# Kernel tuning notes

Hardware: AMD Instinct MI355X
Metric: run time of the kernel (lower is better)

The kernel has to match this reference:

```python
import jax, jax.numpy as jnp
import numpy as np
import math

D_MODEL = 768
NUM_HEADS = 12
D_K = D_MODEL // NUM_HEADS
B, S = 4, 2048


def setup_inputs() -> dict:
    key = jax.random.key(0)
    ks = jax.random.split(key, 11)
    s = 1.0 / math.sqrt(D_MODEL)
    inp = {
        "q": jax.random.normal(ks[0], (B, S, D_MODEL), jnp.float32),
        "k": jax.random.normal(ks[1], (B, S, D_MODEL), jnp.float32),
        "v": jax.random.normal(ks[2], (B, S, D_MODEL), jnp.float32),
        "w_q": jax.random.normal(ks[3], (D_MODEL, D_MODEL), jnp.float32) * s,
        "b_q": jax.random.normal(ks[4], (D_MODEL,), jnp.float32) * s,
        "w_k": jax.random.normal(ks[5], (D_MODEL, D_MODEL), jnp.float32) * s,
        "b_k": jax.random.normal(ks[6], (D_MODEL,), jnp.float32) * s,
        "w_v": jax.random.normal(ks[7], (D_MODEL, D_MODEL), jnp.float32) * s,
        "b_v": jax.random.normal(ks[8], (D_MODEL,), jnp.float32) * s,
        "w_o": jax.random.normal(ks[9], (D_MODEL, D_MODEL), jnp.float32) * s,
        "b_o": jax.random.normal(ks[10], (D_MODEL,), jnp.float32) * s,
    }
    return inp


def reference(q, k, v, w_q, b_q, w_k, b_k, w_v, b_v, w_o, b_o):
    b = q.shape[0]
    # Linear projections (torch Linear: x @ W.T + b), reshape to [B,H,S,d_k]
    def proj(x, w, bias):
        y = x @ w.T + bias
        return y.reshape(b, -1, NUM_HEADS, D_K).transpose(0, 2, 1, 3)

    qh = proj(q, w_q, b_q)
    kh = proj(k, w_k, b_k)
    vh = proj(v, w_v, b_v)

    scale = 1.0 / math.sqrt(D_K)
    scores = jnp.einsum("bhqd,bhkd->bhqk", qh, kh) * scale  # [B,H,S,S]
    attn = jax.nn.softmax(scores, axis=-1)
    # dropout is identity in eval mode
    out = jnp.einsum("bhqk,bhkd->bhqd", attn, vh)
    out = out.transpose(0, 2, 1, 3).reshape(b, -1, D_MODEL)
    return out @ w_o.T + b_o
```

## Files before the change

### kernel.cpp

```cpp
#include <hip/hip_runtime.h>

#define DEV __device__ __forceinline__

typedef __attribute__((ext_vector_type(8))) short short8;
typedef __attribute__((ext_vector_type(4))) float f32x4;
typedef unsigned short u16;
typedef unsigned int u32;

DEV f32x4 mfma16(short8 a, short8 b, f32x4 c) {
    return __builtin_amdgcn_mfma_f32_16x16x32_bf16(a, b, c, 0, 0, 0);
}

DEV u16 f2bf(float f) {
    unsigned u = __builtin_bit_cast(unsigned, f);
    u += 0x7fffu + ((u >> 16) & 1u);
    return (u16)(u >> 16);
}

DEV u32 cvt_pk_bf16(float a, float b) {
    u32 r;
    asm("v_cvt_pk_bf16_f32 %0, %1, %2" : "=v"(r) : "v"(a), "v"(b));
    return r;
}

DEV float fexp2_scaled(float xs) {
    int i = (int)xs + 1065055420;
    return __builtin_bit_cast(float, i);
}

DEV void gload16(const void* g, const void* l) {
    __builtin_amdgcn_global_load_lds(
        (const __attribute__((address_space(1))) unsigned int*)g,
        (__attribute__((address_space(3))) unsigned int*)l, 16, 0, 0);
}

template<int N> DEV void waitvm_barrier() {
    asm volatile("s_waitcnt vmcnt(%0)\n\ts_barrier" :: "n"(N) : "memory");
}

DEV short8 lds_frag_swz(const u16* base, int row, int chunk) {
    int sc = chunk ^ (row & 7);
    return *(const short8*)((const char*)base + row * 128 + sc * 16);
}

__global__ __launch_bounds__(256) void prep(
    const float* __restrict__ q, const float* __restrict__ k, const float* __restrict__ v,
    const float* __restrict__ wq, const float* __restrict__ wk,
    const float* __restrict__ wv, const float* __restrict__ wo,
    u16* __restrict__ xq, u16* __restrict__ xk, u16* __restrict__ xv,
    u16* __restrict__ wqB, u16* __restrict__ wkB, u16* __restrict__ wvB,
    u16* __restrict__ woB)
{
    int b = blockIdx.x;
    const float* s;
    u16* d;
    int i;
    if (b < 18432) {
        int t = b / 6144, r = b % 6144;
        s = t == 0 ? q : t == 1 ? k : v;
        d = t == 0 ? xq : t == 1 ? xk : xv;
        i = r * 256 + threadIdx.x;
    } else {
        int t = (b - 18432) / 576, r = (b - 18432) % 576;
        s = t == 0 ? wq : t == 1 ? wk : t == 2 ? wv : wo;
        d = t == 0 ? wqB : t == 1 ? wkB : t == 2 ? wvB : woB;
        i = r * 256 + threadIdx.x;
    }
    float4 vv = ((const float4*)s)[i];
    ((ushort4*)d)[i] = make_ushort4(f2bf(vv.x), f2bf(vv.y), f2bf(vv.z), f2bf(vv.w));
}

template<int MODE>
DEV void gemm_body(const u16* __restrict__ A_g, const u16* __restrict__ B_g,
                   const float* __restrict__ bias, float scale,
                   u16* __restrict__ outP, float* __restrict__ outF,
                   int mBase, int nBase)
{
    __shared__ u16 AS[64 * 64], BS[128 * 64];

    const int tid = threadIdx.x;
    const int l = tid & 63, wid = tid >> 6;
    const int wy = wid >> 1, wx = wid & 1;
    const int lr = l & 15, lg = l >> 4;

    f32x4 acc[2][4];
    for (int i = 0; i < 2; ++i)
        for (int j = 0; j < 4; ++j) acc[i][j] = (f32x4)0.0f;

    for (int kt = 0; kt < 12; ++kt) {
        if (kt) __syncthreads();
        for (int r = 0; r < 2; ++r) {
            int c = tid + r * 256;
            int row = c >> 3;
            int sc = (c & 7) ^ (row & 7);
            size_t gA = (size_t)(mBase + row) * 768 + kt * 64 + sc * 8;
            gload16(A_g + gA, AS + (size_t)(r * 256 + wid * 64) * 8);
        }
        for (int r = 0; r < 4; ++r) {
            int c = tid + r * 256;
            int row = c >> 3;
            int sc = (c & 7) ^ (row & 7);
            size_t gB = (size_t)(nBase + row) * 768 + kt * 64 + sc * 8;
            gload16(B_g + gB, BS + (size_t)(r * 256 + wid * 64) * 8);
        }
        __syncthreads();

        short8 bf[4][2];
        for (int nt = 0; nt < 4; ++nt)
            for (int ks = 0; ks < 2; ++ks)
                bf[nt][ks] = lds_frag_swz(BS, wx * 64 + nt * 16 + lr, ks * 4 + lg);
        for (int mt = 0; mt < 2; ++mt) {
            short8 ah[2];
            for (int ks = 0; ks < 2; ++ks)
                ah[ks] = lds_frag_swz(AS, wy * 32 + mt * 16 + lr, ks * 4 + lg);
            for (int nt = 0; nt < 4; ++nt)
                for (int ks = 0; ks < 2; ++ks)
                    acc[mt][nt] = mfma16(ah[ks], bf[nt][ks], acc[mt][nt]);
        }
    }

    for (int mt = 0; mt < 2; ++mt)
        for (int nt = 0; nt < 4; ++nt) {
            int colg = nBase + wx * 64 + nt * 16 + lr;
            for (int r = 0; r < 4; ++r) {
                int rowg = mBase + wy * 32 + mt * 16 + lg * 4 + r;
                float bv = (MODE == 2) ? bias[rowg] : bias[colg];
                float vv = (acc[mt][nt][r] + bv) * scale;
                if constexpr (MODE == 0) {
                    int b = rowg >> 11, s = rowg & 2047;
                    int h = colg >> 6, d = colg & 63;
                    outP[((size_t)(b * 12 + h) * 2048 + s) * 64 + d] = f2bf(vv);
                } else if constexpr (MODE == 1) {
                    outF[(size_t)rowg * 768 + colg] = vv;
                } else {
                    int b = colg >> 11, s = colg & 2047;
                    int h = rowg >> 6, d = rowg & 63;
                    outP[((size_t)(b * 12 + h) * 64 + d) * 2048 + s] = f2bf(vv);
                }
            }
        }
}

__global__ __launch_bounds__(256, 4) void gemm_proj(
    const u16* __restrict__ xq, const u16* __restrict__ xk, const u16* __restrict__ xv,
    const u16* __restrict__ wqB, const u16* __restrict__ wkB, const u16* __restrict__ wvB,
    const float* __restrict__ bq, const float* __restrict__ bk, const float* __restrict__ bv,
    u16* __restrict__ Qpl, u16* __restrict__ Kpl, u16* __restrict__ Vtp)
{
    int z = blockIdx.z;
    if (z == 0) {
        gemm_body<0>(xq, wqB, bq, 0.125f * 1.44269504f * 8388608.0f, Qpl, nullptr,
                     blockIdx.y * 64, blockIdx.x * 128);
    } else if (z == 1) {
        gemm_body<0>(xk, wkB, bk, 1.0f, Kpl, nullptr,
                     blockIdx.y * 64, blockIdx.x * 128);
    } else {
        int id = blockIdx.y * 6 + blockIdx.x;
        gemm_body<2>(wvB, xv, bv, 1.0f, Vtp, nullptr,
                     (id % 12) * 64, (id / 12) * 128);
    }
}

__global__ __launch_bounds__(256, 4) void gemm_out(
    const u16* __restrict__ Op, const u16* __restrict__ woB,
    const float* __restrict__ bias, float* __restrict__ outF)
{
    gemm_body<1>(Op, woB, bias, 1.0f, nullptr, outF,
                 blockIdx.y * 64, blockIdx.x * 128);
}

__global__ __launch_bounds__(256, 4) void attn4(
    const u16* __restrict__ Qp, const u16* __restrict__ Kp,
    const u16* __restrict__ Vtp, u16* __restrict__ Op)
{
    __shared__ u16 Ks[2][64 * 64], Vs[2][64 * 64];
    __shared__ u16 Eh[128 * 64];

    const int tid = threadIdx.x;
    const int l = tid & 63, wid = tid >> 6;
    const int lr = l & 15, lg = l >> 4;
    const int bh = blockIdx.x, qt = blockIdx.y;

    short8 q_h[2][2];
    for (int s = 0; s < 2; ++s) {
        size_t qrow = ((size_t)bh * 2048 + qt * 128 + wid * 32 + s * 16 + lr) * 64;
        q_h[s][0] = *(const short8*)(Qp + qrow + lg * 8);
        q_h[s][1] = *(const short8*)(Qp + qrow + 32 + lg * 8);
    }

    short8 ones;
    for (int j = 0; j < 8; ++j) ones[j] = (short)0x3F80;

    f32x4 num[2][4];
    for (int s = 0; s < 2; ++s)
        for (int nt = 0; nt < 4; ++nt) num[s][nt] = (f32x4)0.0f;
    f32x4 denacc[2] = {(f32x4)0.0f, (f32x4)0.0f};

    auto stageK = [&](int kb, int p) {
        for (int r = 0; r < 2; ++r) {
            int c = tid + r * 256;
            int row = c >> 3, sc = (c & 7) ^ (row & 7);
            size_t g = ((size_t)bh * 2048 + kb * 64 + row) * 64 + sc * 8;
            gload16(Kp + g, Ks[p] + (size_t)(r * 256 + wid * 64) * 8);
        }
    };
    auto stageV = [&](int kb, int p) {
        for (int r = 0; r < 2; ++r) {
            int c = tid + r * 256;
            int row = c >> 3, sc = (c & 7) ^ (row & 7);
            size_t g = ((size_t)bh * 64 + row) * 2048 + kb * 64 + sc * 8;
            gload16(Vtp + g, Vs[p] + (size_t)(r * 256 + wid * 64) * 8);
        }
    };

    stageK(0, 0);
    stageV(0, 0);

    for (int kb = 0; kb < 32; ++kb) {
        const int p = kb & 1;
        waitvm_barrier<0>();
        if (kb < 31) {
            stageK(kb + 1, p ^ 1);
            stageV(kb + 1, p ^ 1);
        }

        f32x4 st[2][4];
        for (int s = 0; s < 2; ++s)
            for (int nt = 0; nt < 4; ++nt) st[s][nt] = (f32x4)0.0f;
        __builtin_amdgcn_s_setprio(1);
        for (int nt = 0; nt < 4; ++nt)
            for (int ks = 0; ks < 2; ++ks) {
                short8 kh = lds_frag_swz(Ks[p], nt * 16 + lr, ks * 4 + lg);
                st[0][nt] = mfma16(kh, q_h[0][ks], st[0][nt]);
                st[1][nt] = mfma16(kh, q_h[1][ks], st[1][nt]);
            }
        __builtin_amdgcn_s_setprio(0);

        for (int s = 0; s < 2; ++s)
            for (int nt = 0; nt < 4; ++nt) {
                u32 pk0 = cvt_pk_bf16(fexp2_scaled(st[s][nt][0]), fexp2_scaled(st[s][nt][1]));
                u32 pk1 = cvt_pk_bf16(fexp2_scaled(st[s][nt][2]), fexp2_scaled(st[s][nt][3]));
                int row = wid * 32 + s * 16 + lr;
                int chunk = (2 * nt + (lg >> 1)) ^ (row & 7);
                char* pb = (char*)Eh + row * 128 + chunk * 16 + (lg & 1) * 8;
                *(uint2*)pb = make_uint2(pk0, pk1);
            }

        short8 e[2][2];
        for (int s = 0; s < 2; ++s)
            for (int ks = 0; ks < 2; ++ks)
                e[s][ks] = lds_frag_swz(Eh, wid * 32 + s * 16 + lr, ks * 4 + lg);
        __builtin_amdgcn_s_setprio(1);
        for (int s = 0; s < 2; ++s) {
            denacc[s] = mfma16(e[s][0], ones, denacc[s]);
            denacc[s] = mfma16(e[s][1], ones, denacc[s]);
        }
        for (int nt = 0; nt < 4; ++nt)
            for (int ks = 0; ks < 2; ++ks) {
                short8 vh = lds_frag_swz(Vs[p], nt * 16 + lr, ks * 4 + lg);
                num[0][nt] = mfma16(e[0][ks], vh, num[0][nt]);
                num[1][nt] = mfma16(e[1][ks], vh, num[1][nt]);
            }
        __builtin_amdgcn_s_setprio(0);
    }

    const int b = bh / 12, h = bh % 12;
    for (int s = 0; s < 2; ++s) {
        float rden[4];
        for (int r = 0; r < 4; ++r) rden[r] = 1.0f / denacc[s][r];
        for (int nt = 0; nt < 4; ++nt)
            for (int r = 0; r < 4; ++r) {
                int srow = qt * 128 + wid * 32 + s * 16 + lg * 4 + r;
                size_t rowg = (size_t)b * 2048 + srow;
                int col = h * 64 + nt * 16 + lr;
                Op[rowg * 768 + col] = f2bf(num[s][nt][r] * rden[r]);
            }
    }
}

extern "C" void kernel_launch(void* const* d_in, const int* in_sizes, int n_in,
                              void* d_out, int out_size, void* d_ws, size_t ws_size,
                              hipStream_t stream)
{
    const float* q   = (const float*)d_in[0];
    const float* k   = (const float*)d_in[1];
    const float* v   = (const float*)d_in[2];
    const float* w_q = (const float*)d_in[3];
    const float* b_q = (const float*)d_in[4];
    const float* w_k = (const float*)d_in[5];
    const float* b_k = (const float*)d_in[6];
    const float* w_v = (const float*)d_in[7];
    const float* b_v = (const float*)d_in[8];
    const float* w_o = (const float*)d_in[9];
    const float* b_o = (const float*)d_in[10];
    float* out = (float*)d_out;

    const size_t PL  = (size_t)48 * 2048 * 64;
    const size_t WPL = (size_t)768 * 768;
    u16* base = (u16*)d_ws;
    u16* xqB = base;
    u16* xkB = base + PL;
    u16* xvB = base + 2 * PL;
    u16* Qpl = base + 3 * PL;
    u16* Kpl = base + 4 * PL;
    u16* Vtp = base + 5 * PL;
    u16* OP  = base + 6 * PL;
    u16* W   = base + 7 * PL;
    u16* wqB = W;
    u16* wkB = W + WPL;
    u16* wvB = W + 2 * WPL;
    u16* woB = W + 3 * WPL;

    dim3 bt(256, 1, 1);
    hipLaunchKernelGGL(prep, dim3(20736), bt, 0, stream,
                       q, k, v, w_q, w_k, w_v, w_o,
                       xqB, xkB, xvB, wqB, wkB, wvB, woB);

    hipLaunchKernelGGL(gemm_proj, dim3(6, 128, 3), bt, 0, stream,
                       xqB, xkB, xvB, wqB, wkB, wvB, b_q, b_k, b_v,
                       Qpl, Kpl, Vtp);

    hipLaunchKernelGGL(attn4, dim3(48, 16), bt, 0, stream,
                       Qpl, Kpl, Vtp, OP);

    hipLaunchKernelGGL(gemm_out, dim3(6, 128), bt, 0, stream,
                       OP, woB, b_o, out);
}
```

Before: 161.8 us.

## Rewrite attention with 32x32 MFMA and register-resident probability fragments

The attention kernel switches from 16x16x32 to 32x32x16 bf16 MFMA tiles. The exponentiated scores are now turned into PV operand fragments in registers with cross-half lane shuffles, so the LDS round-trip through the Eh buffer is gone. The softmax denominator is summed in VALU instead of MFMAs against a ones vector. Launch bounds drop to 3 blocks per CU to allow for the larger accumulators, which can lower occupancy and adds shuffle and VALU add work per tile.

```diff
diff --git a/kernel.cpp b/kernel.cpp
--- a/kernel.cpp
+++ b/kernel.cpp
@@ -4,11 +4,16 @@
 
 typedef __attribute__((ext_vector_type(8))) short short8;
 typedef __attribute__((ext_vector_type(4))) float f32x4;
+typedef __attribute__((ext_vector_type(16))) float f32x16;
+typedef __attribute__((ext_vector_type(4))) unsigned int u32x4;
 typedef unsigned short u16;
 typedef unsigned int u32;
 
 DEV f32x4 mfma16(short8 a, short8 b, f32x4 c) {
     return __builtin_amdgcn_mfma_f32_16x16x32_bf16(a, b, c, 0, 0, 0);
+}
+DEV f32x16 mfma32(short8 a, short8 b, f32x16 c) {
+    return __builtin_amdgcn_mfma_f32_32x32x16_bf16(a, b, c, 0, 0, 0);
 }
 
 DEV u16 f2bf(float f) {
@@ -169,32 +174,57 @@
                  blockIdx.y * 64, blockIdx.x * 128);
 }
 
-__global__ __launch_bounds__(256, 4) void attn4(
+template<int C>
+DEV short8 make_efrag(const f32x16& st0, const f32x16& st1, float& den, int hi)
+{
+    constexpr int R = (C & 1) * 8;
+    float e0, e1, e2, e3, e4, e5, e6, e7;
+    if constexpr (C < 2) {
+        e0 = fexp2_scaled(st0[R + 0]); e1 = fexp2_scaled(st0[R + 1]);
+        e2 = fexp2_scaled(st0[R + 2]); e3 = fexp2_scaled(st0[R + 3]);
+        e4 = fexp2_scaled(st0[R + 4]); e5 = fexp2_scaled(st0[R + 5]);
+        e6 = fexp2_scaled(st0[R + 6]); e7 = fexp2_scaled(st0[R + 7]);
+    } else {
+        e0 = fexp2_scaled(st1[R + 0]); e1 = fexp2_scaled(st1[R + 1]);
+        e2 = fexp2_scaled(st1[R + 2]); e3 = fexp2_scaled(st1[R + 3]);
+        e4 = fexp2_scaled(st1[R + 4]); e5 = fexp2_scaled(st1[R + 5]);
+        e6 = fexp2_scaled(st1[R + 6]); e7 = fexp2_scaled(st1[R + 7]);
+    }
+    den += ((e0 + e1) + (e2 + e3)) + ((e4 + e5) + (e6 + e7));
+    u32 pkL0 = cvt_pk_bf16(e0, e1), pkL1 = cvt_pk_bf16(e2, e3);
+    u32 pkH0 = cvt_pk_bf16(e4, e5), pkH1 = cvt_pk_bf16(e6, e7);
+    u32 s0 = hi ? pkL0 : pkH0;
+    u32 s1 = hi ? pkL1 : pkH1;
+    u32 r0 = (u32)__shfl_xor((int)s0, 32, 64);
+    u32 r1 = (u32)__shfl_xor((int)s1, 32, 64);
+    u32x4 f;
+    f.x = hi ? r0 : pkL0;
+    f.y = hi ? r1 : pkL1;
+    f.z = hi ? pkH0 : r0;
+    f.w = hi ? pkH1 : r1;
+    return __builtin_bit_cast(short8, f);
+}
+
+__global__ __launch_bounds__(256, 3) void attn32(
     const u16* __restrict__ Qp, const u16* __restrict__ Kp,
     const u16* __restrict__ Vtp, u16* __restrict__ Op)
 {
     __shared__ u16 Ks[2][64 * 64], Vs[2][64 * 64];
-    __shared__ u16 Eh[128 * 64];
 
     const int tid = threadIdx.x;
     const int l = tid & 63, wid = tid >> 6;
-    const int lr = l & 15, lg = l >> 4;
+    const int lq = l & 31, hi = l >> 5;
     const int bh = blockIdx.x, qt = blockIdx.y;
 
-    short8 q_h[2][2];
-    for (int s = 0; s < 2; ++s) {
-        size_t qrow = ((size_t)bh * 2048 + qt * 128 + wid * 32 + s * 16 + lr) * 64;
-        q_h[s][0] = *(const short8*)(Qp + qrow + lg * 8);
-        q_h[s][1] = *(const short8*)(Qp + qrow + 32 + lg * 8);
-    }
-
-    short8 ones;
-    for (int j = 0; j < 8; ++j) ones[j] = (short)0x3F80;
-
-    f32x4 num[2][4];
-    for (int s = 0; s < 2; ++s)
-        for (int nt = 0; nt < 4; ++nt) num[s][nt] = (f32x4)0.0f;
-    f32x4 denacc[2] = {(f32x4)0.0f, (f32x4)0.0f};
+    short8 q_f[4];
+    {
+        size_t qrow = ((size_t)bh * 2048 + qt * 128 + wid * 32 + lq) * 64;
+        for (int c = 0; c < 4; ++c)
+            q_f[c] = *(const short8*)(Qp + qrow + c * 16 + hi * 8);
+    }
+
+    f32x16 num0 = (f32x16)0.0f, num1 = (f32x16)0.0f;
+    float den_own = 0.0f;
 
     auto stageK = [&](int kb, int p) {
         for (int r = 0; r < 2; ++r) {
@@ -224,57 +254,52 @@
             stageV(kb + 1, p ^ 1);
         }
 
-        f32x4 st[2][4];
-        for (int s = 0; s < 2; ++s)
-            for (int nt = 0; nt < 4; ++nt) st[s][nt] = (f32x4)0.0f;
+        f32x16 st0 = (f32x16)0.0f, st1 = (f32x16)0.0f;
         __builtin_amdgcn_s_setprio(1);
-        for (int nt = 0; nt < 4; ++nt)
-            for (int ks = 0; ks < 2; ++ks) {
-                short8 kh = lds_frag_swz(Ks[p], nt * 16 + lr, ks * 4 + lg);
-                st[0][nt] = mfma16(kh, q_h[0][ks], st[0][nt]);
-                st[1][nt] = mfma16(kh, q_h[1][ks], st[1][nt]);
-            }
+        for (int c = 0; c < 4; ++c) {
+            short8 k0 = lds_frag_swz(Ks[p], lq,      c * 2 + hi);
+            short8 k1 = lds_frag_swz(Ks[p], 32 + lq, c * 2 + hi);
+            st0 = mfma32(k0, q_f[c], st0);
+            st1 = mfma32(k1, q_f[c], st1);
+        }
         __builtin_amdgcn_s_setprio(0);
 
-        for (int s = 0; s < 2; ++s)
-            for (int nt = 0; nt < 4; ++nt) {
-                u32 pk0 = cvt_pk_bf16(fexp2_scaled(st[s][nt][0]), fexp2_scaled(st[s][nt][1]));
-                u32 pk1 = cvt_pk_bf16(fexp2_scaled(st[s][nt][2]), fexp2_scaled(st[s][nt][3]));
-                int row = wid * 32 + s * 16 + lr;
-                int chunk = (2 * nt + (lg >> 1)) ^ (row & 7);
-                char* pb = (char*)Eh + row * 128 + chunk * 16 + (lg & 1) * 8;
-                *(uint2*)pb = make_uint2(pk0, pk1);
-            }
-
-        short8 e[2][2];
-        for (int s = 0; s < 2; ++s)
-            for (int ks = 0; ks < 2; ++ks)
-                e[s][ks] = lds_frag_swz(Eh, wid * 32 + s * 16 + lr, ks * 4 + lg);
+        short8 ef0 = make_efrag<0>(st0, st1, den_own, hi);
+        short8 ef1 = make_efrag<1>(st0, st1, den_own, hi);
+        short8 ef2 = make_efrag<2>(st0, st1, den_own, hi);
+        short8 ef3 = make_efrag<3>(st0, st1, den_own, hi);
+
         __builtin_amdgcn_s_setprio(1);
-        for (int s = 0; s < 2; ++s) {
-            denacc[s] = mfma16(e[s][0], ones, denacc[s]);
-            denacc[s] = mfma16(e[s][1], ones, denacc[s]);
-        }
-        for (int nt = 0; nt < 4; ++nt)
-            for (int ks = 0; ks < 2; ++ks) {
-                short8 vh = lds_frag_swz(Vs[p], nt * 16 + lr, ks * 4 + lg);
-                num[0][nt] = mfma16(e[0][ks], vh, num[0][nt]);
-                num[1][nt] = mfma16(e[1][ks], vh, num[1][nt]);
-            }
+        {
+            short8 v0, v1;
+            v0 = lds_frag_swz(Vs[p], lq,      0 + hi);
+            v1 = lds_frag_swz(Vs[p], 32 + lq, 0 + hi);
+            num0 = mfma32(v0, ef0, num0);
+            num1 = mfma32(v1, ef0, num1);
+            v0 = lds_frag_swz(Vs[p], lq,      2 + hi);
+            v1 = lds_frag_swz(Vs[p], 32 + lq, 2 + hi);
+            num0 = mfma32(v0, ef1, num0);
+            num1 = mfma32(v1, ef1, num1);
+            v0 = lds_frag_swz(Vs[p], lq,      4 + hi);
+            v1 = lds_frag_swz(Vs[p], 32 + lq, 4 + hi);
+            num0 = mfma32(v0, ef2, num0);
+            num1 = mfma32(v1, ef2, num1);
+            v0 = lds_frag_swz(Vs[p], lq,      6 + hi);
+            v1 = lds_frag_swz(Vs[p], 32 + lq, 6 + hi);
+            num0 = mfma32(v0, ef3, num0);
+            num1 = mfma32(v1, ef3, num1);
+        }
         __builtin_amdgcn_s_setprio(0);
     }
 
+    float den = den_own + __shfl_xor(den_own, 32, 64);
+    float rden = 1.0f / den;
     const int b = bh / 12, h = bh % 12;
-    for (int s = 0; s < 2; ++s) {
-        float rden[4];
-        for (int r = 0; r < 4; ++r) rden[r] = 1.0f / denacc[s][r];
-        for (int nt = 0; nt < 4; ++nt)
-            for (int r = 0; r < 4; ++r) {
-                int srow = qt * 128 + wid * 32 + s * 16 + lg * 4 + r;
-                size_t rowg = (size_t)b * 2048 + srow;
-                int col = h * 64 + nt * 16 + lr;
-                Op[rowg * 768 + col] = f2bf(num[s][nt][r] * rden[r]);
-            }
+    size_t rowg = (size_t)b * 2048 + qt * 128 + wid * 32 + lq;
+    for (int r = 0; r < 16; ++r) {
+        int d = (r & 3) + 8 * (r >> 2) + 4 * hi;
+        Op[rowg * 768 + h * 64 + d]      = f2bf(num0[r] * rden);
+        Op[rowg * 768 + h * 64 + 32 + d] = f2bf(num1[r] * rden);
     }
 }
 
@@ -320,7 +345,7 @@
                        xqB, xkB, xvB, wqB, wkB, wvB, b_q, b_k, b_v,
                        Qpl, Kpl, Vtp);
 
-    hipLaunchKernelGGL(attn4, dim3(48, 16), bt, 0, stream,
+    hipLaunchKernelGGL(attn32, dim3(48, 16), bt, 0, stream,
                        Qpl, Kpl, Vtp, OP);
 
     hipLaunchKernelGGL(gemm_out, dim3(6, 128), bt, 0, stream,
```

After: 161.0 us. No clear change (-0.5%).
